# Kernel optimization log

Hardware: AMD Instinct MI355X
Metric: run time of the kernel (lower is better)

The kernel has to match this reference:

```python
import jax, jax.numpy as jnp
import numpy as np

N = 50000       # nodes
E_RAND = 800000 # random edges (avg degree 16); self loops appended
IN, HID, H, OUT = 256, 64, 4, 256
NEG_SLOPE = 0.2


def setup_inputs() -> dict:
    key = jax.random.key(0)
    ks = jax.random.split(key, 8)
    x = jax.random.normal(ks[0], (N, IN), dtype=jnp.float32)
    er = jax.random.randint(ks[1], (2, E_RAND), 0, N, dtype=jnp.int32)
    loops = jnp.arange(N, dtype=jnp.int32)
    edge_index = jnp.concatenate([er, jnp.stack([loops, loops])], axis=1)  # [2, E_RAND+N]
    # xavier-ish scaled params
    W1 = jax.random.normal(ks[2], (H * HID, IN), jnp.float32) * (2.0 / (IN + H * HID)) ** 0.5
    a1_src = jax.random.normal(ks[3], (H, HID), jnp.float32) * 0.1
    a1_dst = jax.random.normal(ks[4], (H, HID), jnp.float32) * 0.1
    W2 = jax.random.normal(ks[5], (OUT, H * HID), jnp.float32) * (2.0 / (H * HID + OUT)) ** 0.5
    a2_src = jax.random.normal(ks[6], (1, OUT), jnp.float32) * 0.1
    a2_dst = jax.random.normal(ks[7], (1, OUT), jnp.float32) * 0.1
    return {"x": x, "edge_index": edge_index, "W1": W1, "a1_src": a1_src,
            "a1_dst": a1_dst, "W2": W2, "a2_src": a2_src, "a2_dst": a2_dst}


def gat_layer(h, W, a_src, a_dst, src, dst, concat):
    n = h.shape[0]
    nh, nf = a_src.shape
    hp = (h @ W.T).reshape(n, nh, nf)                 # [N,H,F]
    e = (hp[src] * a_src).sum(-1) + (hp[dst] * a_dst).sum(-1)  # [E,H]
    e = jnp.where(e > 0, e, NEG_SLOPE * e)            # leaky_relu
    e_max = jax.ops.segment_max(e, dst, num_segments=n)
    ex = jnp.exp(e - e_max[dst])
    e_sum = jax.ops.segment_sum(ex, dst, num_segments=n)
    alpha = ex / (e_sum[dst] + 1e-16)                 # [E,H]
    out = jax.ops.segment_sum(hp[src] * alpha[..., None], dst, num_segments=n)
    return out.reshape(n, nh * nf) if concat else out.mean(axis=1)


def reference(x, edge_index, W1, a1_src, a1_dst, W2, a2_src, a2_dst):
    src, dst = edge_index[0], edge_index[1]
    h = jax.nn.relu(gat_layer(x, W1, a1_src, a1_dst, src, dst, True))
    return gat_layer(h, W2, a2_src, a2_dst, src, dst, False)
```

## Files before the change

### kernel.cpp

```cpp
#include <hip/hip_runtime.h>
#include <math.h>


typedef __attribute__((ext_vector_type(8))) short short8;
typedef __attribute__((ext_vector_type(8))) unsigned short ushort8;
typedef __attribute__((ext_vector_type(4))) float f32x4;
typedef _Float16 half8 __attribute__((ext_vector_type(8)));

__device__ inline unsigned short f2h(float f) {
    _Float16 h = (_Float16)f;
    unsigned short u;
    __builtin_memcpy(&u, &h, 2);
    return u;
}
__device__ inline float h2f(unsigned short u) {
    _Float16 h;
    __builtin_memcpy(&h, &u, 2);
    return (float)h;
}

__global__ void convert_w2(const float* __restrict__ WA, const float* __restrict__ WB,
                           unsigned short* __restrict__ DA, unsigned short* __restrict__ DB) {
    const bool second = blockIdx.x >= 32;
    const float* S = second ? WB : WA;
    unsigned short* D = second ? DB : DA;
    long i = ((long)(blockIdx.x & 31) * 256 + threadIdx.x) * 8;
    float4 v0 = *(const float4*)&S[i];
    float4 v1 = *(const float4*)&S[i + 4];
    ushort8 o;
    o[0] = f2h(v0.x); o[1] = f2h(v0.y); o[2] = f2h(v0.z); o[3] = f2h(v0.w);
    o[4] = f2h(v1.x); o[5] = f2h(v1.y); o[6] = f2h(v1.z); o[7] = f2h(v1.w);
    *(ushort8*)&D[i] = o;
}

template <bool AF32>
__global__ __launch_bounds__(256) void gemm_mfma(const void* __restrict__ A_gv,
                                                 const unsigned short* __restrict__ B_g,
                                                 unsigned short* __restrict__ C, int M) {
    __shared__ unsigned short Ah[64 * 40];
    __shared__ unsigned short Bh[256 * 40];
    const int tid = threadIdx.x;
    const int m0 = blockIdx.x * 64;
    const int w = tid >> 6, lane = tid & 63;
    const int l15 = lane & 15, q = lane >> 4;

    f32x4 acc[16];
    #pragma unroll
    for (int nt = 0; nt < 16; ++nt) acc[nt] = (f32x4){0.f, 0.f, 0.f, 0.f};

    const int ar = tid >> 2;
    const int ak = (tid & 3) * 8;

    for (int k0 = 0; k0 < 256; k0 += 32) {
        int gm = m0 + ar;
        ushort8 aval;
        if (gm < M) {
            if constexpr (AF32) {
                const float* A_g = (const float*)A_gv;
                const float* ap = &A_g[(size_t)gm * 256 + k0 + ak];
                float4 v0 = *(const float4*)(ap);
                float4 v1 = *(const float4*)(ap + 4);
                aval[0] = f2h(v0.x); aval[1] = f2h(v0.y);
                aval[2] = f2h(v0.z); aval[3] = f2h(v0.w);
                aval[4] = f2h(v1.x); aval[5] = f2h(v1.y);
                aval[6] = f2h(v1.z); aval[7] = f2h(v1.w);
            } else {
                const unsigned short* A_g = (const unsigned short*)A_gv;
                aval = *(const ushort8*)&A_g[(size_t)gm * 256 + k0 + ak];
            }
        } else {
            aval = (ushort8){0, 0, 0, 0, 0, 0, 0, 0};
        }
        *(ushort8*)&Ah[ar * 40 + ak] = aval;
        {
            const unsigned short* b0 = &B_g[(size_t)tid * 256 + k0];
            *(ushort8*)&Bh[tid * 40 + 0]  = *(const ushort8*)(b0);
            *(ushort8*)&Bh[tid * 40 + 8]  = *(const ushort8*)(b0 + 8);
            *(ushort8*)&Bh[tid * 40 + 16] = *(const ushort8*)(b0 + 16);
            *(ushort8*)&Bh[tid * 40 + 24] = *(const ushort8*)(b0 + 24);
        }
        __syncthreads();
        int rowA = w * 16 + l15;
        half8 a = *(half8*)&Ah[rowA * 40 + q * 8];
        #pragma unroll
        for (int nt = 0; nt < 16; ++nt) {
            int rowB = nt * 16 + l15;
            half8 bf = *(half8*)&Bh[rowB * 40 + q * 8];
            acc[nt] = __builtin_amdgcn_mfma_f32_16x16x32_f16(a, bf, acc[nt], 0, 0, 0);
        }
        __syncthreads();
    }
    #pragma unroll
    for (int nt = 0; nt < 16; ++nt) {
        #pragma unroll
        for (int r = 0; r < 4; ++r) {
            int gm = m0 + w * 16 + q * 4 + r;
            if (gm < M) C[(size_t)gm * 256 + nt * 16 + l15] = f2h(acc[nt][r]);
        }
    }
}

__global__ void zero_int(int* __restrict__ p, int n) {
    int i = blockIdx.x * 256 + threadIdx.x;
    if (i < n) p[i] = 0;
}

__global__ void hist_kernel(const int* __restrict__ dst, int* __restrict__ deg, int E) {
    int i = blockIdx.x * 256 + threadIdx.x;
    if (i < E) atomicAdd(&deg[dst[i]], 1);
}

__global__ __launch_bounds__(1024) void scan1(const int* __restrict__ deg,
                                              int* __restrict__ lex,
                                              int* __restrict__ bsums, int n) {
    __shared__ int sh[1024];
    int tid = threadIdx.x;
    int i = blockIdx.x * 1024 + tid;
    int v = (i < n) ? deg[i] : 0;
    sh[tid] = v;
    __syncthreads();
    #pragma unroll
    for (int off = 1; off < 1024; off <<= 1) {
        int t2 = (tid >= off) ? sh[tid - off] : 0;
        __syncthreads();
        sh[tid] += t2;
        __syncthreads();
    }
    if (i < n) lex[i] = sh[tid] - v;
    if (tid == 1023) bsums[blockIdx.x] = sh[1023];
}

__global__ __launch_bounds__(1024) void scan23(int* __restrict__ offs,
                                               int* __restrict__ cur,
                                               const int* __restrict__ bsums,
                                               int n, int nb) {
    __shared__ int s_boff, s_total;
    int tid = threadIdx.x;
    if (tid < 64) {
        int bv = (tid < nb) ? bsums[tid] : 0;
        int v = bv;
        #pragma unroll
        for (int off = 1; off < 64; off <<= 1) {
            int t = __shfl_up(v, off, 64);
            if (tid >= off) v += t;
        }
        int incl_bid = __shfl(v, blockIdx.x, 64);
        int bv_bid   = __shfl(bv, blockIdx.x, 64);
        int total    = __shfl(v, nb - 1, 64);
        if (tid == 0) {
            s_boff = incl_bid - bv_bid;
            s_total = total;
        }
    }
    __syncthreads();
    int i = blockIdx.x * 1024 + tid;
    if (i < n) {
        int o = offs[i] + s_boff;
        offs[i] = o;
        cur[i] = o;
    }
    if (blockIdx.x == 0 && tid == 0) offs[n] = s_total;
}

__global__ void scatter_kernel(const int* __restrict__ src, const int* __restrict__ dst,
                               int* __restrict__ cur, int* __restrict__ sorted, int E) {
    int i = blockIdx.x * 256 + threadIdx.x;
    if (i < E) {
        int p = atomicAdd(&cur[dst[i]], 1);
        sorted[p] = src[i];
    }
}

__global__ __launch_bounds__(256) void sort_csr(const int* __restrict__ offs,
                                                int* __restrict__ sorted, int N) {
    const int w = threadIdx.x >> 6, lane = threadIdx.x & 63;
    const int node = blockIdx.x * 4 + w;
    if (node >= N) return;
    const int b = offs[node], e = offs[node + 1];
    const int deg = e - b;
    if (deg < 2 || deg > 64) return;
    int key = (lane < deg) ? sorted[b + lane] : 0x7FFFFFFF;
    #pragma unroll
    for (int k = 2; k <= 64; k <<= 1) {
        #pragma unroll
        for (int j = k >> 1; j > 0; j >>= 1) {
            int other = __shfl_xor(key, j, 64);
            bool keepMin = ((lane & j) == 0) == ((lane & k) == 0);
            int mn = min(key, other), mh = max(key, other);
            key = keepMin ? mn : mh;
        }
    }
    if (lane < deg) sorted[b + lane] = key;
}

template <int NH>
__global__ __launch_bounds__(256) void scompute(const unsigned short* __restrict__ hp,
                                                const float* __restrict__ a_src,
                                                const float* __restrict__ a_dst,
                                                float* __restrict__ s_src,
                                                float* __restrict__ s_dst, int N) {
    const int w = threadIdx.x >> 6, lane = threadIdx.x & 63;
    const int node = blockIdx.x * 4 + w;
    if (node >= N) return;
    const int f0 = lane * 4;
    ushort4 uv = *(const ushort4*)(hp + (size_t)node * 256 + f0);
    float4 as = *(const float4*)(a_src + f0);
    float4 ad = *(const float4*)(a_dst + f0);
    float x0 = h2f(uv.x), x1 = h2f(uv.y), x2 = h2f(uv.z), x3 = h2f(uv.w);
    float p1 = x0 * as.x + x1 * as.y + x2 * as.z + x3 * as.w;
    float p2 = x0 * ad.x + x1 * ad.y + x2 * ad.z + x3 * ad.w;
    if constexpr (NH == 4) {
        #pragma unroll
        for (int off = 1; off < 16; off <<= 1) {
            p1 += __shfl_xor(p1, off, 64);
            p2 += __shfl_xor(p2, off, 64);
        }
        if ((lane & 15) == 0) {
            s_src[node * 4 + (lane >> 4)] = p1;
            s_dst[node * 4 + (lane >> 4)] = p2;
        }
    } else {
        #pragma unroll
        for (int off = 1; off < 64; off <<= 1) {
            p1 += __shfl_xor(p1, off, 64);
            p2 += __shfl_xor(p2, off, 64);
        }
        if (lane == 0) {
            s_src[node] = p1;
            s_dst[node] = p2;
        }
    }
}

template <int NH, bool RELU, bool F16OUT>
__global__ __launch_bounds__(256) void aggregate4(const unsigned short* __restrict__ hp,
                                                  const float* __restrict__ ssrc,
                                                  const float* __restrict__ sdst,
                                                  const int* __restrict__ offs,
                                                  const int* __restrict__ sorted,
                                                  float* __restrict__ out,
                                                  unsigned short* __restrict__ outh, int N) {
    __shared__ int   s_sh[4][64];
    __shared__ float p_sh[4][64][NH];

    const int w = threadIdx.x >> 6, lane = threadIdx.x & 63;
    const int node_raw = blockIdx.x * 4 + w;
    const bool node_ok = node_raw < N;
    const int node = node_ok ? node_raw : (N - 1);
    constexpr int NF = 256 / NH;

    const int b = offs[node], e = offs[node + 1];
    const int deg = e - b;

    float sv[NH];
    #pragma unroll
    for (int h = 0; h < NH; ++h) sv[h] = sdst[node * NH + h];

    float lv[NH], mx[NH];
    const bool small = (deg <= 64);

    if (small) {
        const bool valid = lane < deg;
        const int mys = valid ? sorted[b + lane] : 0;

        float evv[NH];
        if constexpr (NH == 4) {
            float4 sa = *(const float4*)&ssrc[(size_t)mys * 4];
            evv[0] = sa.x + sv[0]; evv[1] = sa.y + sv[1];
            evv[2] = sa.z + sv[2]; evv[3] = sa.w + sv[3];
        } else {
            evv[0] = ssrc[mys] + sv[0];
        }
        #pragma unroll
        for (int h = 0; h < NH; ++h) {
            float ev = evv[h];
            ev = ev > 0.f ? ev : 0.2f * ev;
            evv[h] = valid ? ev : -INFINITY;
            mx[h] = evv[h];
        }
        #pragma unroll
        for (int off = 32; off > 0; off >>= 1)
            #pragma unroll
            for (int h = 0; h < NH; ++h)
                mx[h] = fmaxf(mx[h], __shfl_xor(mx[h], off, 64));

        float pv[NH];
        #pragma unroll
        for (int h = 0; h < NH; ++h) {
            pv[h] = valid ? __expf(evv[h] - mx[h]) : 0.f;
            lv[h] = pv[h];
        }
        #pragma unroll
        for (int off = 32; off > 0; off >>= 1)
            #pragma unroll
            for (int h = 0; h < NH; ++h)
                lv[h] += __shfl_xor(lv[h], off, 64);

        s_sh[w][lane] = mys;
        #pragma unroll
        for (int h = 0; h < NH; ++h) p_sh[w][lane][h] = pv[h];
    } else {
        #pragma unroll
        for (int h = 0; h < NH; ++h) mx[h] = -INFINITY;
        for (int c = b + lane; c < e; c += 64) {
            int s = sorted[c];
            #pragma unroll
            for (int h = 0; h < NH; ++h) {
                float ev = ssrc[s * NH + h] + sv[h];
                ev = ev > 0.f ? ev : 0.2f * ev;
                mx[h] = fmaxf(mx[h], ev);
            }
        }
        #pragma unroll
        for (int off = 32; off > 0; off >>= 1)
            #pragma unroll
            for (int h = 0; h < NH; ++h)
                mx[h] = fmaxf(mx[h], __shfl_xor(mx[h], off, 64));
    }

    __syncthreads();

    if (small) {
        const int quarter = lane >> 4;
        const int l16 = lane & 15;
        const int f0 = l16 * 16;
        const int head = f0 / NF;

        float acc[16];
        #pragma unroll
        for (int k = 0; k < 16; ++k) acc[k] = 0.f;

        const int iters = (deg + 3) >> 2;
        for (int t2 = 0; t2 < iters; ++t2) {
            int j = 4 * t2 + quarter;
            bool jv = j < deg;
            int jj = jv ? j : 0;
            int s = s_sh[w][jj];
            float p = jv ? p_sh[w][jj][head] : 0.f;
            const unsigned short* row = hp + (size_t)s * 256 + f0;
            half8 v0 = *(const half8*)(row);
            half8 v1 = *(const half8*)(row + 8);
            #pragma unroll
            for (int k = 0; k < 8; ++k) {
                acc[k]     = fmaf(p, (float)v0[k], acc[k]);
                acc[8 + k] = fmaf(p, (float)v1[k], acc[8 + k]);
            }
        }
        #pragma unroll
        for (int k = 0; k < 16; ++k) {
            acc[k] += __shfl_xor(acc[k], 16, 64);
            acc[k] += __shfl_xor(acc[k], 32, 64);
        }
        if (node_ok && lane < 16) {
            float li = 1.0f / (lv[head] + 1e-16f);
            float o[16];
            #pragma unroll
            for (int k = 0; k < 16; ++k) {
                o[k] = acc[k] * li;
                if (RELU) o[k] = fmaxf(o[k], 0.f);
            }
            if constexpr (F16OUT) {
                ushort8 u0, u1;
                #pragma unroll
                for (int k = 0; k < 8; ++k) {
                    u0[k] = f2h(o[k]);
                    u1[k] = f2h(o[8 + k]);
                }
                *(ushort8*)&outh[(size_t)node * 256 + f0]     = u0;
                *(ushort8*)&outh[(size_t)node * 256 + f0 + 8] = u1;
            } else {
                float* op = &out[(size_t)node * 256 + f0];
                *(float4*)&op[0]  = make_float4(o[0], o[1], o[2], o[3]);
                *(float4*)&op[4]  = make_float4(o[4], o[5], o[6], o[7]);
                *(float4*)&op[8]  = make_float4(o[8], o[9], o[10], o[11]);
                *(float4*)&op[12] = make_float4(o[12], o[13], o[14], o[15]);
            }
        }
    } else {
        const int half = lane >> 5;
        const int l32 = lane & 31;
        const int f0 = l32 * 8;
        const int head = f0 / NF;

        float acc[8];
        #pragma unroll
        for (int k = 0; k < 8; ++k) acc[k] = 0.f;
        #pragma unroll
        for (int h = 0; h < NH; ++h) lv[h] = 0.f;

        int last = -1, round = 0;
        for (;;) {
            int myMin = 0x7FFFFFFF, myCnt = 0;
            for (int c = b + lane; c < e; c += 64) {
                int s = sorted[c];
                if (s > last) {
                    if (s < myMin) { myMin = s; myCnt = 1; }
                    else if (s == myMin) ++myCnt;
                }
            }
            #pragma unroll
            for (int off = 32; off > 0; off >>= 1) {
                int om = __shfl_xor(myMin, off, 64);
                int oc = __shfl_xor(myCnt, off, 64);
                if (om < myMin) { myMin = om; myCnt = oc; }
                else if (om == myMin) myCnt += oc;
            }
            if (myMin == 0x7FFFFFFF) break;
            const bool mine = ((round & 1) == half);
            float cf = (float)myCnt;
            float ph[NH];
            #pragma unroll
            for (int h = 0; h < NH; ++h) {
                float ev = ssrc[myMin * NH + h] + sv[h];
                ev = ev > 0.f ? ev : 0.2f * ev;
                ph[h] = __expf(ev - mx[h]);
            }
            if (mine && l32 == 0) {
                #pragma unroll
                for (int h = 0; h < NH; ++h) lv[h] += cf * ph[h];
            }
            if (mine) {
                float p = cf * ph[head];
                half8 v = *(const half8*)(hp + (size_t)myMin * 256 + f0);
                #pragma unroll
                for (int k = 0; k < 8; ++k) acc[k] = fmaf(p, (float)v[k], acc[k]);
            }
            last = myMin; ++round;
        }
        #pragma unroll
        for (int off = 32; off > 0; off >>= 1)
            #pragma unroll
            for (int h = 0; h < NH; ++h)
                lv[h] += __shfl_xor(lv[h], off, 64);

        #pragma unroll
        for (int k = 0; k < 8; ++k) acc[k] += __shfl_xor(acc[k], 32, 64);

        if (node_ok && lane < 32) {
            float li = 1.0f / (lv[head] + 1e-16f);
            float o[8];
            #pragma unroll
            for (int k = 0; k < 8; ++k) {
                o[k] = acc[k] * li;
                if (RELU) o[k] = fmaxf(o[k], 0.f);
            }
            if constexpr (F16OUT) {
                ushort8 u0;
                #pragma unroll
                for (int k = 0; k < 8; ++k) u0[k] = f2h(o[k]);
                *(ushort8*)&outh[(size_t)node * 256 + f0] = u0;
            } else {
                *(float4*)&out[(size_t)node * 256 + f0]     = make_float4(o[0], o[1], o[2], o[3]);
                *(float4*)&out[(size_t)node * 256 + f0 + 4] = make_float4(o[4], o[5], o[6], o[7]);
            }
        }
    }
}

extern "C" void kernel_launch(void* const* d_in, const int* in_sizes, int n_in,
                              void* d_out, int out_size, void* d_ws, size_t ws_size,
                              hipStream_t stream) {
    const float* x   = (const float*)d_in[0];
    const int*   ei  = (const int*)d_in[1];
    const float* W1  = (const float*)d_in[2];
    const float* a1s = (const float*)d_in[3];
    const float* a1d = (const float*)d_in[4];
    const float* W2  = (const float*)d_in[5];
    const float* a2s = (const float*)d_in[6];
    const float* a2d = (const float*)d_in[7];
    float* out = (float*)d_out;

    const int N = in_sizes[0] / 256;
    const int E = in_sizes[1] / 2;
    const int* src = ei;
    const int* dst = ei + E;

    unsigned short* hp = (unsigned short*)d_ws;
    float* ssrc  = (float*)(hp + (size_t)N * 256);
    float* sdst  = ssrc + (size_t)N * 4;
    int*   deg   = (int*)(sdst + (size_t)N * 4);
    int*   cur   = deg + N;
    int*   offs  = cur + N;
    int*   sorted= offs + N + 1;
    int*   bsums = sorted + E;
    int*   boffs = bsums + 64;
    unsigned short* w1h = (unsigned short*)(boffs + 64);
    unsigned short* w2h = w1h + 65536;

    unsigned short* hh = (unsigned short*)d_out;

    const int nb = (N + 1023) / 1024;

    convert_w2<<<64, 256, 0, stream>>>(W1, W2, w1h, w2h);

    zero_int<<<(N + 255) / 256, 256, 0, stream>>>(deg, N);
    hist_kernel<<<(E + 255) / 256, 256, 0, stream>>>(dst, deg, E);
    scan1<<<nb, 1024, 0, stream>>>(deg, offs, bsums, N);
    scan23<<<nb, 1024, 0, stream>>>(offs, cur, bsums, N, nb);
    scatter_kernel<<<(E + 255) / 256, 256, 0, stream>>>(src, dst, cur, sorted, E);

    int gemmblocks = (N + 63) / 64;
    int aggblocks = (N + 3) / 4;
    sort_csr<<<aggblocks, 256, 0, stream>>>(offs, sorted, N);

    gemm_mfma<true><<<gemmblocks, 256, 0, stream>>>(x, w1h, hp, N);
    scompute<4><<<aggblocks, 256, 0, stream>>>(hp, a1s, a1d, ssrc, sdst, N);
    aggregate4<4, true, true><<<aggblocks, 256, 0, stream>>>(hp, ssrc, sdst, offs, sorted,
                                                             nullptr, hh, N);

    gemm_mfma<false><<<gemmblocks, 256, 0, stream>>>(hh, w2h, hp, N);
    scompute<1><<<aggblocks, 256, 0, stream>>>(hp, a2s, a2d, ssrc, sdst, N);
    aggregate4<1, false, false><<<aggblocks, 256, 0, stream>>>(hp, ssrc, sdst, offs, sorted,
                                                               out, nullptr, N);
}
```

Before: 415.1 us.

## Fuse attention score computation into MFMA GEMM epilogue and merge prep kernels

Computes the per-node source/destination attention scores directly from the fp32 GEMM accumulators in the epilogue, which removes the separate scompute kernels and their re-read of hp. The GEMM tile also grows from 64 to 128 rows, with 512 threads arranged as a 4x2 wave grid so each wave does 2x8 MFMA tiles, raising A/B fragment reuse. The weight conversion and degree zeroing are merged into one prep kernel to save a launch. Scores are now taken from fp32 accumulators rather than fp16-rounded values, which changes numerics slightly. The larger tile adds register pressure and halves the number of blocks.

```diff
diff --git a/kernel.cpp b/kernel.cpp
--- a/kernel.cpp
+++ b/kernel.cpp
@@ -2,7 +2,6 @@
 #include <math.h>
 
 
-typedef __attribute__((ext_vector_type(8))) short short8;
 typedef __attribute__((ext_vector_type(8))) unsigned short ushort8;
 typedef __attribute__((ext_vector_type(4))) float f32x4;
 typedef _Float16 half8 __attribute__((ext_vector_type(8)));
@@ -19,37 +18,51 @@
     return (float)h;
 }
 
-__global__ void convert_w2(const float* __restrict__ WA, const float* __restrict__ WB,
-                           unsigned short* __restrict__ DA, unsigned short* __restrict__ DB) {
-    const bool second = blockIdx.x >= 32;
-    const float* S = second ? WB : WA;
-    unsigned short* D = second ? DB : DA;
-    long i = ((long)(blockIdx.x & 31) * 256 + threadIdx.x) * 8;
-    float4 v0 = *(const float4*)&S[i];
-    float4 v1 = *(const float4*)&S[i + 4];
-    ushort8 o;
-    o[0] = f2h(v0.x); o[1] = f2h(v0.y); o[2] = f2h(v0.z); o[3] = f2h(v0.w);
-    o[4] = f2h(v1.x); o[5] = f2h(v1.y); o[6] = f2h(v1.z); o[7] = f2h(v1.w);
-    *(ushort8*)&D[i] = o;
-}
-
-template <bool AF32>
-__global__ __launch_bounds__(256) void gemm_mfma(const void* __restrict__ A_gv,
-                                                 const unsigned short* __restrict__ B_g,
-                                                 unsigned short* __restrict__ C, int M) {
-    __shared__ unsigned short Ah[64 * 40];
+__global__ void prep(const float* __restrict__ WA, const float* __restrict__ WB,
+                     unsigned short* __restrict__ DA, unsigned short* __restrict__ DB,
+                     int* __restrict__ deg, int N) {
+    int i = blockIdx.x * 256 + threadIdx.x;
+    if (i < N) deg[i] = 0;
+    if (blockIdx.x < 64) {
+        const bool second = blockIdx.x >= 32;
+        const float* S = second ? WB : WA;
+        unsigned short* D = second ? DB : DA;
+        long j = ((long)(blockIdx.x & 31) * 256 + threadIdx.x) * 8;
+        float4 v0 = *(const float4*)&S[j];
+        float4 v1 = *(const float4*)&S[j + 4];
+        ushort8 o;
+        o[0] = f2h(v0.x); o[1] = f2h(v0.y); o[2] = f2h(v0.z); o[3] = f2h(v0.w);
+        o[4] = f2h(v1.x); o[5] = f2h(v1.y); o[6] = f2h(v1.z); o[7] = f2h(v1.w);
+        *(ushort8*)&D[j] = o;
+    }
+}
+
+template <bool AF32, int NH>
+__global__ __launch_bounds__(512) void gemm_sc(const void* __restrict__ A_gv,
+                                               const unsigned short* __restrict__ B_g,
+                                               unsigned short* __restrict__ C,
+                                               const float* __restrict__ a_src,
+                                               const float* __restrict__ a_dst,
+                                               float* __restrict__ s_src,
+                                               float* __restrict__ s_dst, int M) {
+    __shared__ unsigned short Ah[128 * 40];
     __shared__ unsigned short Bh[256 * 40];
     const int tid = threadIdx.x;
-    const int m0 = blockIdx.x * 64;
+    const int m0 = blockIdx.x * 128;
     const int w = tid >> 6, lane = tid & 63;
+    const int wm = w >> 1, wn = w & 1;
     const int l15 = lane & 15, q = lane >> 4;
 
-    f32x4 acc[16];
+    f32x4 acc[2][8];
     #pragma unroll
-    for (int nt = 0; nt < 16; ++nt) acc[nt] = (f32x4){0.f, 0.f, 0.f, 0.f};
+    for (int mt = 0; mt < 2; ++mt)
+        #pragma unroll
+        for (int nt = 0; nt < 8; ++nt) acc[mt][nt] = (f32x4){0.f, 0.f, 0.f, 0.f};
 
     const int ar = tid >> 2;
     const int ak = (tid & 3) * 8;
+    const int br = tid >> 1;
+    const int bk = (tid & 1) * 16;
 
     for (int k0 = 0; k0 < 256; k0 += 32) {
         int gm = m0 + ar;
@@ -73,36 +86,123 @@
         }
         *(ushort8*)&Ah[ar * 40 + ak] = aval;
         {
-            const unsigned short* b0 = &B_g[(size_t)tid * 256 + k0];
-            *(ushort8*)&Bh[tid * 40 + 0]  = *(const ushort8*)(b0);
-            *(ushort8*)&Bh[tid * 40 + 8]  = *(const ushort8*)(b0 + 8);
-            *(ushort8*)&Bh[tid * 40 + 16] = *(const ushort8*)(b0 + 16);
-            *(ushort8*)&Bh[tid * 40 + 24] = *(const ushort8*)(b0 + 24);
+            const unsigned short* b0 = &B_g[(size_t)br * 256 + k0 + bk];
+            *(ushort8*)&Bh[br * 40 + bk]     = *(const ushort8*)(b0);
+            *(ushort8*)&Bh[br * 40 + bk + 8] = *(const ushort8*)(b0 + 8);
         }
         __syncthreads();
-        int rowA = w * 16 + l15;
-        half8 a = *(half8*)&Ah[rowA * 40 + q * 8];
-        #pragma unroll
-        for (int nt = 0; nt < 16; ++nt) {
-            int rowB = nt * 16 + l15;
+        half8 a[2];
+        #pragma unroll
+        for (int mt = 0; mt < 2; ++mt) {
+            int rowA = wm * 32 + mt * 16 + l15;
+            a[mt] = *(half8*)&Ah[rowA * 40 + q * 8];
+        }
+        #pragma unroll
+        for (int nt = 0; nt < 8; ++nt) {
+            int rowB = wn * 128 + nt * 16 + l15;
             half8 bf = *(half8*)&Bh[rowB * 40 + q * 8];
-            acc[nt] = __builtin_amdgcn_mfma_f32_16x16x32_f16(a, bf, acc[nt], 0, 0, 0);
+            #pragma unroll
+            for (int mt = 0; mt < 2; ++mt)
+                acc[mt][nt] = __builtin_amdgcn_mfma_f32_16x16x32_f16(a[mt], bf, acc[mt][nt], 0, 0, 0);
         }
         __syncthreads();
     }
+
     #pragma unroll
-    for (int nt = 0; nt < 16; ++nt) {
-        #pragma unroll
-        for (int r = 0; r < 4; ++r) {
-            int gm = m0 + w * 16 + q * 4 + r;
-            if (gm < M) C[(size_t)gm * 256 + nt * 16 + l15] = f2h(acc[nt][r]);
-        }
-    }
-}
-
-__global__ void zero_int(int* __restrict__ p, int n) {
-    int i = blockIdx.x * 256 + threadIdx.x;
-    if (i < n) p[i] = 0;
+    for (int mt = 0; mt < 2; ++mt) {
+        #pragma unroll
+        for (int nt = 0; nt < 8; ++nt) {
+            #pragma unroll
+            for (int r = 0; r < 4; ++r) {
+                int gm = m0 + wm * 32 + mt * 16 + q * 4 + r;
+                if (gm < M) C[(size_t)gm * 256 + wn * 128 + nt * 16 + l15] = f2h(acc[mt][nt][r]);
+            }
+        }
+    }
+
+    float as[8], ad[8];
+    #pragma unroll
+    for (int nt = 0; nt < 8; ++nt) {
+        int col = wn * 128 + nt * 16 + l15;
+        as[nt] = a_src[col];
+        ad[nt] = a_dst[col];
+    }
+
+    if constexpr (NH == 4) {
+        #pragma unroll
+        for (int mt = 0; mt < 2; ++mt) {
+            #pragma unroll
+            for (int r = 0; r < 4; ++r) {
+                float s0 = 0.f, s1 = 0.f, d0 = 0.f, d1 = 0.f;
+                #pragma unroll
+                for (int nt = 0; nt < 4; ++nt) {
+                    s0 = fmaf(acc[mt][nt][r], as[nt], s0);
+                    d0 = fmaf(acc[mt][nt][r], ad[nt], d0);
+                }
+                #pragma unroll
+                for (int nt = 4; nt < 8; ++nt) {
+                    s1 = fmaf(acc[mt][nt][r], as[nt], s1);
+                    d1 = fmaf(acc[mt][nt][r], ad[nt], d1);
+                }
+                #pragma unroll
+                for (int off = 1; off < 16; off <<= 1) {
+                    s0 += __shfl_xor(s0, off, 64);
+                    s1 += __shfl_xor(s1, off, 64);
+                    d0 += __shfl_xor(d0, off, 64);
+                    d1 += __shfl_xor(d1, off, 64);
+                }
+                int gm = m0 + wm * 32 + mt * 16 + q * 4 + r;
+                if (l15 == 0 && gm < M) {
+                    s_src[gm * 4 + 2 * wn + 0] = s0;
+                    s_src[gm * 4 + 2 * wn + 1] = s1;
+                    s_dst[gm * 4 + 2 * wn + 0] = d0;
+                    s_dst[gm * 4 + 2 * wn + 1] = d1;
+                }
+            }
+        }
+    } else {
+        float* part = (float*)Ah;
+        float ss[8], dd[8];
+        #pragma unroll
+        for (int mt = 0; mt < 2; ++mt) {
+            #pragma unroll
+            for (int r = 0; r < 4; ++r) {
+                float s = 0.f, d = 0.f;
+                #pragma unroll
+                for (int nt = 0; nt < 8; ++nt) {
+                    s = fmaf(acc[mt][nt][r], as[nt], s);
+                    d = fmaf(acc[mt][nt][r], ad[nt], d);
+                }
+                #pragma unroll
+                for (int off = 1; off < 16; off <<= 1) {
+                    s += __shfl_xor(s, off, 64);
+                    d += __shfl_xor(d, off, 64);
+                }
+                ss[mt * 4 + r] = s;
+                dd[mt * 4 + r] = d;
+                int rloc = wm * 32 + mt * 16 + q * 4 + r;
+                if (wn == 1 && l15 == 0) {
+                    part[rloc * 2]     = s;
+                    part[rloc * 2 + 1] = d;
+                }
+            }
+        }
+        __syncthreads();
+        if (wn == 0) {
+            #pragma unroll
+            for (int mt = 0; mt < 2; ++mt) {
+                #pragma unroll
+                for (int r = 0; r < 4; ++r) {
+                    int rloc = wm * 32 + mt * 16 + q * 4 + r;
+                    int gm = m0 + rloc;
+                    if (l15 == 0 && gm < M) {
+                        s_src[gm] = ss[mt * 4 + r] + part[rloc * 2];
+                        s_dst[gm] = dd[mt * 4 + r] + part[rloc * 2 + 1];
+                    }
+                }
+            }
+        }
+    }
 }
 
 __global__ void hist_kernel(const int* __restrict__ dst, int* __restrict__ deg, int E) {
@@ -193,45 +293,6 @@
     if (lane < deg) sorted[b + lane] = key;
 }
 
-template <int NH>
-__global__ __launch_bounds__(256) void scompute(const unsigned short* __restrict__ hp,
-                                                const float* __restrict__ a_src,
-                                                const float* __restrict__ a_dst,
-                                                float* __restrict__ s_src,
-                                                float* __restrict__ s_dst, int N) {
-    const int w = threadIdx.x >> 6, lane = threadIdx.x & 63;
-    const int node = blockIdx.x * 4 + w;
-    if (node >= N) return;
-    const int f0 = lane * 4;
-    ushort4 uv = *(const ushort4*)(hp + (size_t)node * 256 + f0);
-    float4 as = *(const float4*)(a_src + f0);
-    float4 ad = *(const float4*)(a_dst + f0);
-    float x0 = h2f(uv.x), x1 = h2f(uv.y), x2 = h2f(uv.z), x3 = h2f(uv.w);
-    float p1 = x0 * as.x + x1 * as.y + x2 * as.z + x3 * as.w;
-    float p2 = x0 * ad.x + x1 * ad.y + x2 * ad.z + x3 * ad.w;
-    if constexpr (NH == 4) {
-        #pragma unroll
-        for (int off = 1; off < 16; off <<= 1) {
-            p1 += __shfl_xor(p1, off, 64);
-            p2 += __shfl_xor(p2, off, 64);
-        }
-        if ((lane & 15) == 0) {
-            s_src[node * 4 + (lane >> 4)] = p1;
-            s_dst[node * 4 + (lane >> 4)] = p2;
-        }
-    } else {
-        #pragma unroll
-        for (int off = 1; off < 64; off <<= 1) {
-            p1 += __shfl_xor(p1, off, 64);
-            p2 += __shfl_xor(p2, off, 64);
-        }
-        if (lane == 0) {
-            s_src[node] = p1;
-            s_dst[node] = p2;
-        }
-    }
-}
-
 template <int NH, bool RELU, bool F16OUT>
 __global__ __launch_bounds__(256) void aggregate4(const unsigned short* __restrict__ hp,
                                                   const float* __restrict__ ssrc,
@@ -490,26 +551,24 @@
     unsigned short* hh = (unsigned short*)d_out;
 
     const int nb = (N + 1023) / 1024;
-
-    convert_w2<<<64, 256, 0, stream>>>(W1, W2, w1h, w2h);
-
-    zero_int<<<(N + 255) / 256, 256, 0, stream>>>(deg, N);
+    const int prepblocks = ((N + 255) / 256) > 64 ? ((N + 255) / 256) : 64;
+
+    prep<<<prepblocks, 256, 0, stream>>>(W1, W2, w1h, w2h, deg, N);
+
     hist_kernel<<<(E + 255) / 256, 256, 0, stream>>>(dst, deg, E);
     scan1<<<nb, 1024, 0, stream>>>(deg, offs, bsums, N);
     scan23<<<nb, 1024, 0, stream>>>(offs, cur, bsums, N, nb);
     scatter_kernel<<<(E + 255) / 256, 256, 0, stream>>>(src, dst, cur, sorted, E);
 
-    int gemmblocks = (N + 63) / 64;
+    int gemmblocks = (N + 127) / 128;
     int aggblocks = (N + 3) / 4;
     sort_csr<<<aggblocks, 256, 0, stream>>>(offs, sorted, N);
 
-    gemm_mfma<true><<<gemmblocks, 256, 0, stream>>>(x, w1h, hp, N);
-    scompute<4><<<aggblocks, 256, 0, stream>>>(hp, a1s, a1d, ssrc, sdst, N);
+    gemm_sc<true, 4><<<gemmblocks, 512, 0, stream>>>(x, w1h, hp, a1s, a1d, ssrc, sdst, N);
     aggregate4<4, true, true><<<aggblocks, 256, 0, stream>>>(hp, ssrc, sdst, offs, sorted,
                                                              nullptr, hh, N);
 
-    gemm_mfma<false><<<gemmblocks, 256, 0, stream>>>(hh, w2h, hp, N);
-    scompute<1><<<aggblocks, 256, 0, stream>>>(hp, a2s, a2d, ssrc, sdst, N);
+    gemm_sc<false, 1><<<gemmblocks, 512, 0, stream>>>(hh, w2h, hp, a2s, a2d, ssrc, sdst, N);
     aggregate4<1, false, false><<<aggblocks, 256, 0, stream>>>(hp, ssrc, sdst, offs, sorted,
                                                                out, nullptr, N);
 }
```

New measurement: 383.0 us. -7.7%, faster.
